# Kernel optimization log

Measured on AMD Instinct MI355X. Metric: run time of the kernel, lower is better.

Reference implementation:

```python
import jax, jax.numpy as jnp
import numpy as np

C = 512
GROUPS = 8
EPS = 1e-5


def setup_inputs() -> dict:
    key = jax.random.key(0)
    ks = jax.random.split(key, 7)
    B, H, W = 16, 32, 32
    x = jax.random.normal(ks[0], (B, C, H, W), dtype=jnp.float32)
    gamma = jnp.ones((C,), jnp.float32)
    beta = jnp.zeros((C,), jnp.float32)
    # 1x1 convs stored as [out, in] matrices
    w_qkv = jax.random.normal(ks[1], (3 * C, C), dtype=jnp.float32) * (1.0 / np.sqrt(C))
    b_qkv = jax.random.normal(ks[2], (3 * C,), dtype=jnp.float32) * 0.02
    w_proj = jax.random.normal(ks[3], (C, C), dtype=jnp.float32) * (1.0 / np.sqrt(C))
    b_proj = jax.random.normal(ks[4], (C,), dtype=jnp.float32) * 0.02
    return {"x": x, "gamma": gamma, "beta": beta, "w_qkv": w_qkv,
            "b_qkv": b_qkv, "w_proj": w_proj, "b_proj": b_proj}


def _group_norm(x, gamma, beta):
    B, Cc, H, W = x.shape
    xg = x.reshape(B, GROUPS, Cc // GROUPS, H, W)
    mean = xg.mean(axis=(2, 3, 4), keepdims=True)
    var = xg.var(axis=(2, 3, 4), keepdims=True)
    xg = (xg - mean) * jax.lax.rsqrt(var + EPS)
    x = xg.reshape(B, Cc, H, W)
    return x * gamma[None, :, None, None] + beta[None, :, None, None]


def reference(x, gamma, beta, w_qkv, b_qkv, w_proj, b_proj):
    B, Cc, H, W = x.shape
    N = H * W
    h = _group_norm(x, gamma, beta)  # [B,C,H,W]
    hf = h.reshape(B, Cc, N)  # [B,C,N]
    # 1x1 conv == matmul over channel dim
    qkv = jnp.einsum('oc,bcn->bon', w_qkv, hf) + b_qkv[None, :, None]  # [B,3C,N]
    q, k, v = jnp.split(qkv, 3, axis=1)  # each [B,C,N]
    scale = 1.0 / jnp.sqrt(jnp.float32(Cc))
    # attn[b,i,j] = sum_c q[b,c,i] * k[b,c,j]
    attn = jnp.einsum('bci,bcj->bij', q, k) * scale  # [B,N,N]
    attn = jax.nn.softmax(attn, axis=-1)
    out = jnp.einsum('bij,bcj->bci', attn, v)  # [B,C,N]
    out = jnp.einsum('oc,bcn->bon', w_proj, out) + b_proj[None, :, None]
    return x + out.reshape(B, Cc, H, W)
```

## Files before the change

kernel.cpp:

```cpp
#include <hip/hip_runtime.h>
#include <hip/hip_bf16.h>

typedef unsigned short u16;
typedef unsigned int u32;
typedef __attribute__((ext_vector_type(8))) short short8;
typedef __attribute__((ext_vector_type(4))) float floatx4;

#define BATCH 16
#define CDIM 512
#define NSPAT 1024
#define NGROUP 8

__device__ __forceinline__ u16 f2bf(float f) {
    unsigned u = __float_as_uint(f);
    u += 0x7FFFu + ((u >> 16) & 1u);
    return (u16)(u >> 16);
}
__device__ __forceinline__ u32 f2bf2(float lo, float hi) {
    __hip_bfloat162 h = __float22bfloat162_rn(make_float2(lo, hi));
    return *(u32*)&h;
}
__device__ __forceinline__ float bf2f(u16 v) {
    u32 t = ((u32)v) << 16;
    return __uint_as_float(t);
}

__device__ __forceinline__ void load_lds16(const void* g, void* l) {
    __builtin_amdgcn_global_load_lds(
        (const __attribute__((address_space(1))) unsigned int*)g,
        (__attribute__((address_space(3))) unsigned int*)l, 16, 0, 0);
}

#define SBAR0 __builtin_amdgcn_sched_barrier(0)
#define BARRIER { SBAR0; __builtin_amdgcn_s_barrier(); SBAR0; }

__global__ __launch_bounds__(256) void prep_kernel(
    const float* __restrict__ w_qkv, const float* __restrict__ w_proj,
    const float* __restrict__ b_qkv, const float* __restrict__ x,
    u16* __restrict__ wproj_bf, u16* __restrict__ wq_t, u16* __restrict__ wk_t,
    u16* __restrict__ wv_t, float* __restrict__ stats, float* __restrict__ lsums,
    float* __restrict__ bpv, float* __restrict__ cvec) {
    int b = blockIdx.x;
    int tid = threadIdx.x;
    if (b < 256) {
        int i = b * 256 + tid;
        float4 v = ((const float4*)w_proj)[i];
        u32* d = (u32*)wproj_bf;
        d[i * 2] = f2bf2(v.x, v.y);
        d[i * 2 + 1] = f2bf2(v.z, v.w);
        return;
    }
    if (b < 448) {
        __shared__ u16 t[64 * 66];
        int bt = b - 256;
        int which = bt >> 6;
        int bt2 = bt & 63;
        int tx = bt2 & 7, ty = bt2 >> 3;
        const float* src = w_qkv + (size_t)(which * 512 + ty * 64) * CDIM + tx * 64;
        u16* dstb = (which == 0) ? wq_t : (which == 1) ? wk_t : wv_t;
#pragma unroll
        for (int p = 0; p < 4; ++p) {
            int r = p * 16 + (tid >> 4);
            int c4 = (tid & 15) << 2;
            float4 v = *(const float4*)(src + (size_t)r * CDIM + c4);
            u16* d = &t[r * 66 + c4];
            d[0] = f2bf(v.x); d[1] = f2bf(v.y); d[2] = f2bf(v.z); d[3] = f2bf(v.w);
        }
        __syncthreads();
        u16* dst = dstb + (size_t)(tx * 64) * CDIM + ty * 64;
#pragma unroll
        for (int p = 0; p < 4; ++p) {
            int c = p * 16 + (tid >> 4);
            int r4 = (tid & 15) << 2;
            ushort4 o;
            o.x = t[(r4 + 0) * 66 + c];
            o.y = t[(r4 + 1) * 66 + c];
            o.z = t[(r4 + 2) * 66 + c];
            o.w = t[(r4 + 3) * 66 + c];
            *(ushort4*)(dst + (size_t)c * CDIM + r4) = o;
        }
        return;
    }
    if (b < 576) {
        __shared__ float rs[4], rss[4];
        int bg = b - 448;
        const float4* xv = (const float4*)(x + (size_t)bg * 65536);
        float s = 0.f, ss = 0.f;
        for (int i = tid; i < 16384; i += 256) {
            float4 v = xv[i];
            s += v.x + v.y + v.z + v.w;
            ss += v.x * v.x + v.y * v.y + v.z * v.z + v.w * v.w;
        }
#pragma unroll
        for (int off = 32; off; off >>= 1) { s += __shfl_down(s, off); ss += __shfl_down(ss, off); }
        int wave = tid >> 6, lane = tid & 63;
        if (lane == 0) { rs[wave] = s; rss[wave] = ss; }
        __syncthreads();
        if (tid == 0) {
            float S1 = rs[0] + rs[1] + rs[2] + rs[3];
            float S2 = rss[0] + rss[1] + rss[2] + rss[3];
            float mean = S1 * (1.f / 65536.f);
            float var = S2 * (1.f / 65536.f) - mean * mean;
            stats[bg * 2] = mean;
            stats[bg * 2 + 1] = rsqrtf(var + 1e-5f);
        }
        return;
    }
    if (b < 592) {
        ((float4*)lsums)[(b - 576) * 256 + tid] = (float4){0.f, 0.f, 0.f, 0.f};
        return;
    }
    if (b < 600) {
        int o0 = (b - 592) * 64;
        int wave = tid >> 6, lane = tid & 63;
        const float4* bvv = (const float4*)(b_qkv + 1024);
        float4 v0 = bvv[lane * 2], v1 = bvv[lane * 2 + 1];
        for (int it = 0; it < 16; ++it) {
            int o = o0 + wave * 16 + it;
            const float4* wr = (const float4*)(w_proj + (size_t)o * CDIM);
            float4 a0 = wr[lane * 2], a1 = wr[lane * 2 + 1];
            float s = a0.x * v0.x + a0.y * v0.y + a0.z * v0.z + a0.w * v0.w
                    + a1.x * v1.x + a1.y * v1.y + a1.z * v1.z + a1.w * v1.w;
#pragma unroll
            for (int off = 32; off; off >>= 1) s += __shfl_down(s, off);
            if (lane == 0) bpv[o] = s;
        }
        return;
    }
    {
        int col = (b - 600) * 256 + tid;
        float s = 0.f;
        for (int m = 0; m < 512; ++m)
            s += w_qkv[(size_t)(512 + m) * CDIM + col] * b_qkv[m];
        cvec[col] = s;
    }
}

__device__ __forceinline__ void stage_tile(
    const u16* __restrict__ Ab, const u16* __restrict__ Bb, int lda, int ldb,
    int m0, int n0, int k0, u16* As, u16* Bs) {
    int tid = threadIdx.x;
#pragma unroll
    for (int it = 0; it < 4; ++it) {
        int c = it * 256 + tid;
        int r = c >> 3, p = c & 7;
        int kc = p ^ (r & 7);
        load_lds16(Ab + (size_t)(m0 + r) * lda + k0 + (kc << 3), &As[c << 3]);
        load_lds16(Bb + (size_t)(n0 + r) * ldb + k0 + (kc << 3), &Bs[c << 3]);
    }
}

__device__ __forceinline__ void compute_tile(
    const u16* As, const u16* Bs, int wm, int wn, int quad, int lrow,
    floatx4 (&acc)[4][4]) {
#pragma unroll
    for (int s = 0; s < 2; ++s) {
        short8 af[4], bf[4];
#pragma unroll
        for (int i = 0; i < 4; ++i) {
            int R = wm + i * 16 + lrow;
            int p = (s * 4 + quad) ^ (R & 7);
            af[i] = *(const short8*)&As[(R << 6) + (p << 3)];
        }
#pragma unroll
        for (int j = 0; j < 4; ++j) {
            int R = wn + j * 16 + lrow;
            int p = (s * 4 + quad) ^ (R & 7);
            bf[j] = *(const short8*)&Bs[(R << 6) + (p << 3)];
        }
#pragma unroll
        for (int i = 0; i < 4; ++i)
#pragma unroll
            for (int j = 0; j < 4; ++j)
                acc[i][j] = __builtin_amdgcn_mfma_f32_16x16x32_bf16(af[i], bf[j], acc[i][j], 0, 0, 0);
    }
}

__device__ __forceinline__ void gemm_core_sb(
    const u16* __restrict__ Ab, const u16* __restrict__ Bb, int K, int lda, int ldb,
    int m0, int n0, u16* As, u16* Bs, floatx4 (&acc)[4][4]) {
    int tid = threadIdx.x;
    int lane = tid & 63, wave = tid >> 6, quad = lane >> 4, lrow = lane & 15;
    int wm = (wave >> 1) << 6, wn = (wave & 1) << 6;
    for (int k0 = 0; k0 < K; k0 += 64) {
        stage_tile(Ab, Bb, lda, ldb, m0, n0, k0, As, Bs);
        __syncthreads();
        compute_tile(As, Bs, wm, wn, quad, lrow, acc);
        __syncthreads();
    }
}

#define ACC_INIT floatx4 acc[4][4]; \
    _Pragma("unroll") for (int i = 0; i < 4; ++i) \
    _Pragma("unroll") for (int j = 0; j < 4; ++j) acc[i][j] = (floatx4){0.f, 0.f, 0.f, 0.f};

#define EPILOG_IDX int lane = threadIdx.x & 63, wave = threadIdx.x >> 6; \
    int quad = lane >> 4, lrow = lane & 15; \
    int wm = (wave >> 1) << 6, wn = (wave & 1) << 6;

__device__ __forceinline__ void issueA2(
    const u16* __restrict__ Ab, int lda, int m0, int t, int h, u16* smem) {
    int tid = threadIdx.x;
    u16* base = smem + (t & 1) * 16384 + h * 8192;
#pragma unroll
    for (int l = 0; l < 2; ++l) {
        int c = l * 512 + tid;
        int rho = c >> 3, p = c & 7;
        int kc = p ^ (rho & 7);
        int r = ((rho >> 6) << 7) | (h << 6) | (rho & 63);
        load_lds16(Ab + (size_t)(m0 + r) * lda + (t << 6) + (kc << 3), base + (c << 3));
    }
}
__device__ __forceinline__ void issueB2(
    const u16* __restrict__ Bb, int ldb, int n0, int t, int h, u16* smem) {
    int tid = threadIdx.x;
    u16* base = smem + 32768 + (t & 1) * 16384 + h * 8192;
#pragma unroll
    for (int l = 0; l < 2; ++l) {
        int c = l * 512 + tid;
        int rho = c >> 3, p = c & 7;
        int kc = p ^ (rho & 7);
        int r = ((rho >> 5) << 6) | (h << 5) | (rho & 31);
        load_lds16(Bb + (size_t)(n0 + r) * ldb + (t << 6) + (kc << 3), base + (c << 3));
    }
}

__device__ __forceinline__ void gemm256x256(
    const u16* __restrict__ Ab, const u16* __restrict__ Bb, int K, int lda, int ldb,
    int m0, int n0, u16* smem, floatx4 (&acc)[8][4]) {
    int tid = threadIdx.x;
    int lane = tid & 63, wave = tid >> 6;
    int quad = lane >> 4, lrow = lane & 15;
    int wrow = wave >> 2, wcol = wave & 3;
    int nt = K >> 6;
    issueA2(Ab, lda, m0, 0, 0, smem);
    issueA2(Ab, lda, m0, 0, 1, smem);
    issueB2(Bb, ldb, n0, 0, 0, smem);
    issueB2(Bb, ldb, n0, 0, 1, smem);
    for (int t = 0; t < nt; ++t) {
        int slot = t & 1;
        BARRIER;
        if (t + 1 < nt) {
            issueA2(Ab, lda, m0, t + 1, 0, smem);
            issueA2(Ab, lda, m0, t + 1, 1, smem);
            issueB2(Bb, ldb, n0, t + 1, 0, smem);
            issueB2(Bb, ldb, n0, t + 1, 1, smem);
            asm volatile("s_waitcnt vmcnt(8)" ::: "memory");
        } else {
            asm volatile("s_waitcnt vmcnt(0)" ::: "memory");
        }
        BARRIER;
        const u16* Ah = smem + slot * 16384;
        const u16* Bh = smem + 32768 + slot * 16384;
        short8 bf[2][4];
#pragma unroll
        for (int qn = 0; qn < 2; ++qn)
#pragma unroll
            for (int ks = 0; ks < 2; ++ks)
#pragma unroll
                for (int j = 0; j < 2; ++j) {
                    int rho = wcol * 32 + j * 16 + lrow;
                    int p = (ks * 4 + quad) ^ (lrow & 7);
                    bf[qn][ks * 2 + j] = *(const short8*)&Bh[qn * 8192 + (rho << 6) + (p << 3)];
                }
#pragma unroll
        for (int qm = 0; qm < 2; ++qm) {
            short8 af[8];
#pragma unroll
            for (int ks = 0; ks < 2; ++ks)
#pragma unroll
                for (int i = 0; i < 4; ++i) {
                    int rho = wrow * 64 + i * 16 + lrow;
                    int p = (ks * 4 + quad) ^ (lrow & 7);
                    af[ks * 4 + i] = *(const short8*)&Ah[qm * 8192 + (rho << 6) + (p << 3)];
                }
#pragma unroll
            for (int ks = 0; ks < 2; ++ks)
#pragma unroll
                for (int i = 0; i < 4; ++i)
#pragma unroll
                    for (int qn = 0; qn < 2; ++qn)
#pragma unroll
                        for (int j = 0; j < 2; ++j)
                            acc[qm * 4 + i][qn * 2 + j] = __builtin_amdgcn_mfma_f32_16x16x32_bf16(
                                af[ks * 4 + i], bf[qn][ks * 2 + j], acc[qm * 4 + i][qn * 2 + j], 0, 0, 0);
        }
    }
}

__device__ __forceinline__ void issueA4(
    const u16* __restrict__ Ab, int lda, int m0, int t, u16* smem) {
    int tid = threadIdx.x;
    u16* base = smem + (t & 1) * 16384;
#pragma unroll
    for (int l = 0; l < 4; ++l) {
        int c = l * 512 + tid;
        int rho = c >> 3, p = c & 7;
        int kc = p ^ (rho & 7);
        load_lds16(Ab + (size_t)(m0 + rho) * lda + (t << 6) + (kc << 3), base + (c << 3));
    }
}
__device__ __forceinline__ void issueB4(
    const u16* __restrict__ Bb, int ldb, int n0, int t, int h, u16* smem) {
    int tid = threadIdx.x;
    u16* base = smem + 32768 + (t & 1) * 8192 + h * 4096;
    int rho = tid >> 3, p = tid & 7;
    int kc = p ^ (rho & 7);
    int r = ((rho >> 5) << 6) | (h << 5) | (rho & 31);
    load_lds16(Bb + (size_t)(n0 + r) * ldb + (t << 6) + (kc << 3), base + (tid << 3));
}

__device__ __forceinline__ void gemm256x128(
    const u16* __restrict__ Ab, const u16* __restrict__ Bb, int K, int lda, int ldb,
    int m0, int n0, u16* smem, floatx4 (&acc)[4][4]) {
    int tid = threadIdx.x;
    int lane = tid & 63, wave = tid >> 6;
    int quad = lane >> 4, lrow = lane & 15;
    int wrow = wave >> 1, wcol = wave & 1;
    int nt = K >> 6;
    issueA4(Ab, lda, m0, 0, smem);
    issueB4(Bb, ldb, n0, 0, 0, smem);
    issueB4(Bb, ldb, n0, 0, 1, smem);
    for (int t = 0; t < nt; ++t) {
        int slot = t & 1;
        BARRIER;
        if (t + 1 < nt) {
            issueA4(Ab, lda, m0, t + 1, smem);
            issueB4(Bb, ldb, n0, t + 1, 0, smem);
            issueB4(Bb, ldb, n0, t + 1, 1, smem);
            asm volatile("s_waitcnt vmcnt(6)" ::: "memory");
        } else {
            asm volatile("s_waitcnt vmcnt(0)" ::: "memory");
        }
        BARRIER;
        const u16* Ah = smem + slot * 16384;
        const u16* Bh = smem + 32768 + slot * 8192;
        short8 bf[2][4];
#pragma unroll
        for (int qn = 0; qn < 2; ++qn)
#pragma unroll
            for (int ks = 0; ks < 2; ++ks)
#pragma unroll
                for (int j = 0; j < 2; ++j) {
                    int rho = wcol * 32 + j * 16 + lrow;
                    int p = (ks * 4 + quad) ^ (lrow & 7);
                    bf[qn][ks * 2 + j] = *(const short8*)&Bh[qn * 4096 + (rho << 6) + (p << 3)];
                }
        short8 af[8];
#pragma unroll
        for (int ks = 0; ks < 2; ++ks)
#pragma unroll
            for (int i = 0; i < 4; ++i) {
                int rho = wrow * 64 + i * 16 + lrow;
                int p = (ks * 4 + quad) ^ (lrow & 7);
                af[ks * 4 + i] = *(const short8*)&Ah[(rho << 6) + (p << 3)];
            }
#pragma unroll
        for (int ks = 0; ks < 2; ++ks)
#pragma unroll
            for (int i = 0; i < 4; ++i)
#pragma unroll
                for (int qn = 0; qn < 2; ++qn)
#pragma unroll
                    for (int j = 0; j < 2; ++j)
                        acc[i][qn * 2 + j] = __builtin_amdgcn_mfma_f32_16x16x32_bf16(
                            af[ks * 4 + i], bf[qn][ks * 2 + j], acc[i][qn * 2 + j], 0, 0, 0);
    }
}

#define ACC_INIT84 floatx4 acc[8][4]; \
    _Pragma("unroll") for (int i = 0; i < 8; ++i) \
    _Pragma("unroll") for (int j = 0; j < 4; ++j) acc[i][j] = (floatx4){0.f, 0.f, 0.f, 0.f};

#define ACC_INIT44 floatx4 acc[4][4]; \
    _Pragma("unroll") for (int i = 0; i < 4; ++i) \
    _Pragma("unroll") for (int j = 0; j < 4; ++j) acc[i][j] = (floatx4){0.f, 0.f, 0.f, 0.f};

#define TSTR 66
__global__ __launch_bounds__(256) void gn_wpv_kernel(
    const float* __restrict__ x, const float* __restrict__ gamma, const float* __restrict__ beta,
    const float* __restrict__ stats, u16* __restrict__ hT,
    const u16* __restrict__ wproj_bf, const u16* __restrict__ wq_t,
    const u16* __restrict__ wk_t, const u16* __restrict__ wv_t, u16* __restrict__ wmega) {
    __shared__ u16 smem[2 * 128 * 64];
    int tid = threadIdx.x;
    if (blockIdx.z == 16) {
        if (blockIdx.x >= 4) return;
        bool isM = blockIdx.y < 4;
        int m0 = (isM ? blockIdx.y : blockIdx.y - 4) << 7;
        int n0 = blockIdx.x << 7;
        const u16* Aop = isM ? wq_t : wproj_bf;
        const u16* Bop = isM ? wk_t : wv_t;
        int rbase = isM ? 0 : 512;
        ACC_INIT;
        gemm_core_sb(Aop, Bop, CDIM, CDIM, CDIM, m0, n0, smem, smem + 128 * 64, acc);
        EPILOG_IDX;
#pragma unroll
        for (int i = 0; i < 4; ++i)
#pragma unroll
            for (int j = 0; j < 4; ++j)
#pragma unroll
                for (int r = 0; r < 4; ++r) {
                    int R = m0 + wm + i * 16 + (quad << 2) + r;
                    int Cc = n0 + wn + j * 16 + lrow;
                    wmega[(size_t)(rbase + R) * CDIM + Cc] = f2bf(acc[i][j][r]);
                }
        return;
    }
    u16* t = smem;
    int b = blockIdx.z, c0 = blockIdx.y << 6, n0 = blockIdx.x << 6;
    const float* xb = x + ((size_t)b * CDIM + c0) * NSPAT + n0;
#pragma unroll
    for (int p = 0; p < 4; ++p) {
        int cl = p * 16 + (tid >> 4);
        int nl = (tid & 15) << 2;
        int c = c0 + cl;
        int bg = b * NGROUP + (c >> 6);
        float ga = gamma[c] * stats[bg * 2 + 1];
        float be = beta[c] - stats[bg * 2] * ga;
        float4 v = *(const float4*)(xb + (size_t)cl * NSPAT + nl);
        u16* dst = &t[cl * TSTR + nl];
        dst[0] = f2bf(v.x * ga + be);
        dst[1] = f2bf(v.y * ga + be);
        dst[2] = f2bf(v.z * ga + be);
        dst[3] = f2bf(v.w * ga + be);
    }
    __syncthreads();
    u16* hb = hT + ((size_t)b * NSPAT + n0) * CDIM + c0;
#pragma unroll
    for (int p = 0; p < 4; ++p) {
        int nl = p * 16 + (tid >> 4);
        int cl4 = (tid & 15) << 2;
        ushort4 o;
        o.x = t[(cl4 + 0) * TSTR + nl];
        o.y = t[(cl4 + 1) * TSTR + nl];
        o.z = t[(cl4 + 2) * TSTR + nl];
        o.w = t[(cl4 + 3) * TSTR + nl];
        *(ushort4*)(hb + (size_t)nl * CDIM + cl4) = o;
    }
}

__global__ __launch_bounds__(512, 2) void qkv_kernel(
    const u16* __restrict__ wmega, const u16* __restrict__ hT,
    const float* __restrict__ cvec, const float* __restrict__ bpv,
    u16* __restrict__ gT, u16* __restrict__ WV, float* __restrict__ rbuf) {
    extern __shared__ u16 smem[];
    int z = blockIdx.x;
    if (blockIdx.y == 4) {
        if (blockIdx.z != 0) return;
        int tid = threadIdx.x;
        const u16* hb = hT + (size_t)z * CDIM * NSPAT;
#pragma unroll 1
        for (int jj = 0; jj < 2; ++jj) {
            int j = tid * 2 + jj;
            const short8* hp = (const short8*)(hb + (size_t)j * CDIM);
            float s = 0.f;
#pragma unroll 4
            for (int cc = 0; cc < 64; ++cc) {
                short8 v = hp[cc];
                const float4* cv = (const float4*)&cvec[cc * 8];
                float4 c0 = cv[0], c1 = cv[1];
                s += c0.x * bf2f((u16)v[0]) + c0.y * bf2f((u16)v[1])
                   + c0.z * bf2f((u16)v[2]) + c0.w * bf2f((u16)v[3])
                   + c1.x * bf2f((u16)v[4]) + c1.y * bf2f((u16)v[5])
                   + c1.z * bf2f((u16)v[6]) + c1.w * bf2f((u16)v[7]);
            }
            rbuf[(size_t)z * NSPAT + j] = s;
        }
        return;
    }
    int n0 = blockIdx.y << 8;
    int m0 = blockIdx.z << 8;
    const u16* Bb = hT + (size_t)z * CDIM * NSPAT;
    ACC_INIT84;
    gemm256x256(wmega, Bb, CDIM, CDIM, CDIM, m0, n0, smem, acc);
    int lane = threadIdx.x & 63, wave = threadIdx.x >> 6;
    int quad = lane >> 4, lrow = lane & 15;
    int wrow = wave >> 2, wcol = wave & 3;
    if (blockIdx.z < 2) {
        u16* gp = gT + (size_t)z * NSPAT * CDIM;
#pragma unroll
        for (int mf = 0; mf < 8; ++mf) {
            int R0 = m0 + wrow * 128 + mf * 16 + (quad << 2);
#pragma unroll
            for (int nf = 0; nf < 4; ++nf) {
                int Cc = n0 + wcol * 64 + nf * 16 + lrow;
                uint2 u;
                u.x = f2bf2(acc[mf][nf][0], acc[mf][nf][1]);
                u.y = f2bf2(acc[mf][nf][2], acc[mf][nf][3]);
                *(uint2*)&gp[(size_t)Cc * CDIM + R0] = u;
            }
        }
    } else {
        u16* Wp = WV + (size_t)z * CDIM * NSPAT;
#pragma unroll
        for (int mf = 0; mf < 8; ++mf) {
            int R = m0 - 512 + wrow * 128 + mf * 16 + (quad << 2);
            float4 pv = *(const float4*)&bpv[R];
#pragma unroll
            for (int nf = 0; nf < 4; ++nf) {
                int Cc = n0 + wcol * 64 + nf * 16 + lrow;
                Wp[(size_t)(R + 0) * NSPAT + Cc] = f2bf(acc[mf][nf][0] + pv.x);
                Wp[(size_t)(R + 1) * NSPAT + Cc] = f2bf(acc[mf][nf][1] + pv.y);
                Wp[(size_t)(R + 2) * NSPAT + Cc] = f2bf(acc[mf][nf][2] + pv.z);
                Wp[(size_t)(R + 3) * NSPAT + Cc] = f2bf(acc[mf][nf][3] + pv.w);
            }
        }
    }
}

__global__ __launch_bounds__(512, 2) void scores_kernel(
    const u16* __restrict__ gT, const u16* __restrict__ hT,
    u16* __restrict__ P, float* __restrict__ lsums, const float* __restrict__ rbuf,
    float scale) {
    extern __shared__ u16 smem[];
    int z = blockIdx.x;
    int n0 = blockIdx.y << 8;
    int m0 = blockIdx.z << 8;
    const u16* gb = gT + (size_t)z * NSPAT * CDIM;
    const u16* hb = hT + (size_t)z * CDIM * NSPAT;
    ACC_INIT84;
    gemm256x256(gb, hb, CDIM, CDIM, CDIM, m0, n0, smem, acc);
    int lane = threadIdx.x & 63, wave = threadIdx.x >> 6;
    int quad = lane >> 4, lrow = lane & 15;
    int wrow = wave >> 2, wcol = wave & 3;
    u16* Pp = P + (size_t)z * NSPAT * NSPAT;
    float* ls = lsums + (size_t)z * NSPAT;
    const float* rb = rbuf + (size_t)z * NSPAT;
#pragma unroll
    for (int nf = 0; nf < 4; ++nf) {
        int Ci = n0 + wcol * 64 + nf * 16 + lrow;
        float part = 0.f;
#pragma unroll
        for (int mf = 0; mf < 8; ++mf) {
            int Rj0 = m0 + wrow * 128 + mf * 16 + (quad << 2);
            float4 rv = *(const float4*)&rb[Rj0];
            float e0 = __expf((acc[mf][nf][0] + rv.x) * scale);
            float e1 = __expf((acc[mf][nf][1] + rv.y) * scale);
            float e2 = __expf((acc[mf][nf][2] + rv.z) * scale);
            float e3 = __expf((acc[mf][nf][3] + rv.w) * scale);
            part += (e0 + e1) + (e2 + e3);
            uint2 u;
            u.x = f2bf2(e0, e1);
            u.y = f2bf2(e2, e3);
            *(uint2*)&Pp[(size_t)Ci * NSPAT + Rj0] = u;
        }
        part += __shfl_xor(part, 16);
        part += __shfl_xor(part, 32);
        if (lane < 16) atomicAdd(&ls[Ci], part);
    }
}

__global__ __launch_bounds__(512, 2) void final_kernel(
    const u16* __restrict__ WV, const u16* __restrict__ P, const float* __restrict__ lsums,
    const float* __restrict__ bias, const float* __restrict__ x, float* __restrict__ out) {
    extern __shared__ u16 smem[];
    int z = blockIdx.x;
    int n0 = blockIdx.y << 7;
    int m0 = blockIdx.z << 8;
    const u16* Pb = P + (size_t)z * NSPAT * NSPAT;
    const u16* WVb = WV + (size_t)z * CDIM * NSPAT;
    ACC_INIT44;
    gemm256x128(Pb, WVb, NSPAT, NSPAT, NSPAT, m0, n0, smem, acc);
    int lane = threadIdx.x & 63, wave = threadIdx.x >> 6;
    int quad = lane >> 4, lrow = lane & 15;
    int wrow = wave >> 1, wcol = wave & 1;
    float* Op = out + (size_t)z * CDIM * NSPAT;
    const float* xr = x + (size_t)z * CDIM * NSPAT;
    const float* li = lsums + (size_t)z * NSPAT;
#pragma unroll
    for (int mf = 0; mf < 4; ++mf) {
        int Ri0 = m0 + wrow * 64 + mf * 16 + (quad << 2);
        float4 lv = *(const float4*)&li[Ri0];
        float s0 = __builtin_amdgcn_rcpf(lv.x);
        float s1 = __builtin_amdgcn_rcpf(lv.y);
        float s2 = __builtin_amdgcn_rcpf(lv.z);
        float s3 = __builtin_amdgcn_rcpf(lv.w);
#pragma unroll
        for (int nf = 0; nf < 4; ++nf) {
            int Co = n0 + wcol * 64 + nf * 16 + lrow;
            float bv = bias[Co];
            size_t off = (size_t)Co * NSPAT + Ri0;
            float4 xv = *(const float4*)&xr[off];
            float4 o;
            o.x = acc[mf][nf][0] * s0 + bv + xv.x;
            o.y = acc[mf][nf][1] * s1 + bv + xv.y;
            o.z = acc[mf][nf][2] * s2 + bv + xv.z;
            o.w = acc[mf][nf][3] * s3 + bv + xv.w;
            *(float4*)&Op[off] = o;
        }
    }
}

extern "C" void kernel_launch(void* const* d_in, const int* in_sizes, int n_in,
                              void* d_out, int out_size, void* d_ws, size_t ws_size,
                              hipStream_t stream) {
    const float* x      = (const float*)d_in[0];
    const float* gamma  = (const float*)d_in[1];
    const float* beta   = (const float*)d_in[2];
    const float* w_qkv  = (const float*)d_in[3];
    const float* b_qkv  = (const float*)d_in[4];
    const float* w_proj = (const float*)d_in[5];
    const float* b_proj = (const float*)d_in[6];
    float* out = (float*)d_out;

    const size_t CN = (size_t)CDIM * NSPAT;
    const size_t NN = (size_t)NSPAT * NSPAT;
    const float SCALE = 0.044194173824159216f;
    const int LDS_BIG = 131072;
    const int LDS_MED = 98304;

    static bool lds_attr_done = false;
    if (!lds_attr_done) {
        hipFuncSetAttribute((const void*)qkv_kernel,
                            hipFuncAttributeMaxDynamicSharedMemorySize, LDS_BIG);
        hipFuncSetAttribute((const void*)scores_kernel,
                            hipFuncAttributeMaxDynamicSharedMemorySize, LDS_BIG);
        hipFuncSetAttribute((const void*)final_kernel,
                            hipFuncAttributeMaxDynamicSharedMemorySize, LDS_MED);
        lds_attr_done = true;
    }

    char* ws = (char*)d_ws;
    float* stats   = (float*)ws;
    float* bpv     = (float*)(ws + 1024);
    float* cvec    = (float*)(ws + 3072);
    u16* wmega     = (u16*)(ws + 8192);
    u16* wproj_bf  = wmega + (size_t)1024 * CDIM;
    u16* wq_t      = wproj_bf + (size_t)CDIM * CDIM;
    u16* wk_t      = wq_t + (size_t)CDIM * CDIM;
    u16* wv_t      = wk_t + (size_t)CDIM * CDIM;
    u16* hT        = wv_t + (size_t)CDIM * CDIM;
    u16* gT        = hT + BATCH * CN;
    u16* WV        = gT + BATCH * CN;
    u16* P         = WV + BATCH * CN;
    float* lsums   = (float*)(P + BATCH * NN);
    float* rbuf    = lsums + (size_t)BATCH * NSPAT;

    prep_kernel<<<602, 256, 0, stream>>>(
        w_qkv, w_proj, b_qkv, x, wproj_bf, wq_t, wk_t, wv_t, stats, lsums, bpv, cvec);

    gn_wpv_kernel<<<dim3(16, 8, 17), 256, 0, stream>>>(
        x, gamma, beta, stats, hT, wproj_bf, wq_t, wk_t, wv_t, wmega);

    qkv_kernel<<<dim3(BATCH, 5, 4), 512, LDS_BIG, stream>>>(
        wmega, hT, cvec, bpv, gT, WV, rbuf);

    scores_kernel<<<dim3(BATCH, 4, 4), 512, LDS_BIG, stream>>>(
        gT, hT, P, lsums, rbuf, SCALE);

    final_kernel<<<dim3(BATCH, 4, 4), 512, LDS_MED, stream>>>(WV, P, lsums, b_proj, x, out);
}
```

Baseline: 136.6 us.

## Fuse rbuf row-bias reduction into group-norm transpose kernel via atomics

Moves the per-position dot product of cvec with the normalized activations out of a dedicated slice of the qkv kernel and into the group-norm/transpose kernel. There it is computed from the bf16 tile already held in shared memory and accumulated into rbuf with atomicAdd. The prep kernel gets extra blocks to zero rbuf alongside lsums. This removes the serial, low-parallelism rbuf blocks from the qkv grid and a second read of hT, at the cost of an extra barrier and global atomics in the transpose kernel. The atomic accumulation order is nondeterministic.

New measurement: 128.8 us. 1.06x faster.

```diff
diff --git a/kernel.cpp b/kernel.cpp
--- a/kernel.cpp
+++ b/kernel.cpp
@@ -106,12 +106,12 @@
         }
         return;
     }
-    if (b < 592) {
+    if (b < 608) {
         ((float4*)lsums)[(b - 576) * 256 + tid] = (float4){0.f, 0.f, 0.f, 0.f};
         return;
     }
-    if (b < 600) {
-        int o0 = (b - 592) * 64;
+    if (b < 616) {
+        int o0 = (b - 608) * 64;
         int wave = tid >> 6, lane = tid & 63;
         const float4* bvv = (const float4*)(b_qkv + 1024);
         float4 v0 = bvv[lane * 2], v1 = bvv[lane * 2 + 1];
@@ -128,7 +128,7 @@
         return;
     }
     {
-        int col = (b - 600) * 256 + tid;
+        int col = (b - 616) * 256 + tid;
         float s = 0.f;
         for (int m = 0; m < 512; ++m)
             s += w_qkv[(size_t)(512 + m) * CDIM + col] * b_qkv[m];
@@ -381,8 +381,10 @@
     const float* __restrict__ x, const float* __restrict__ gamma, const float* __restrict__ beta,
     const float* __restrict__ stats, u16* __restrict__ hT,
     const u16* __restrict__ wproj_bf, const u16* __restrict__ wq_t,
-    const u16* __restrict__ wk_t, const u16* __restrict__ wv_t, u16* __restrict__ wmega) {
+    const u16* __restrict__ wk_t, const u16* __restrict__ wv_t, u16* __restrict__ wmega,
+    const float* __restrict__ cvec, float* __restrict__ rbuf) {
     __shared__ u16 smem[2 * 128 * 64];
+    __shared__ float rp[4][64];
     int tid = threadIdx.x;
     if (blockIdx.z == 16) {
         if (blockIdx.x >= 4) return;
@@ -426,6 +428,21 @@
         dst[3] = f2bf(v.w * ga + be);
     }
     __syncthreads();
+    {
+        int j = tid & 63, part = tid >> 6;
+        float rs_ = 0.f;
+#pragma unroll
+        for (int q = 0; q < 16; ++q) {
+            int cl = part * 16 + q;
+            rs_ += cvec[c0 + cl] * bf2f(t[cl * TSTR + j]);
+        }
+        rp[part][j] = rs_;
+    }
+    __syncthreads();
+    if (tid < 64) {
+        float s = rp[0][tid] + rp[1][tid] + rp[2][tid] + rp[3][tid];
+        atomicAdd(&rbuf[(size_t)b * NSPAT + n0 + tid], s);
+    }
     u16* hb = hT + ((size_t)b * NSPAT + n0) * CDIM + c0;
 #pragma unroll
     for (int p = 0; p < 4; ++p) {
@@ -442,33 +459,10 @@
 
 __global__ __launch_bounds__(512, 2) void qkv_kernel(
     const u16* __restrict__ wmega, const u16* __restrict__ hT,
-    const float* __restrict__ cvec, const float* __restrict__ bpv,
-    u16* __restrict__ gT, u16* __restrict__ WV, float* __restrict__ rbuf) {
+    const float* __restrict__ bpv,
+    u16* __restrict__ gT, u16* __restrict__ WV) {
     extern __shared__ u16 smem[];
     int z = blockIdx.x;
-    if (blockIdx.y == 4) {
-        if (blockIdx.z != 0) return;
-        int tid = threadIdx.x;
-        const u16* hb = hT + (size_t)z * CDIM * NSPAT;
-#pragma unroll 1
-        for (int jj = 0; jj < 2; ++jj) {
-            int j = tid * 2 + jj;
-            const short8* hp = (const short8*)(hb + (size_t)j * CDIM);
-            float s = 0.f;
-#pragma unroll 4
-            for (int cc = 0; cc < 64; ++cc) {
-                short8 v = hp[cc];
-                const float4* cv = (const float4*)&cvec[cc * 8];
-                float4 c0 = cv[0], c1 = cv[1];
-                s += c0.x * bf2f((u16)v[0]) + c0.y * bf2f((u16)v[1])
-                   + c0.z * bf2f((u16)v[2]) + c0.w * bf2f((u16)v[3])
-                   + c1.x * bf2f((u16)v[4]) + c1.y * bf2f((u16)v[5])
-                   + c1.z * bf2f((u16)v[6]) + c1.w * bf2f((u16)v[7]);
-            }
-            rbuf[(size_t)z * NSPAT + j] = s;
-        }
-        return;
-    }
     int n0 = blockIdx.y << 8;
     int m0 = blockIdx.z << 8;
     const u16* Bb = hT + (size_t)z * CDIM * NSPAT;
@@ -637,14 +631,14 @@
     float* lsums   = (float*)(P + BATCH * NN);
     float* rbuf    = lsums + (size_t)BATCH * NSPAT;
 
-    prep_kernel<<<602, 256, 0, stream>>>(
+    prep_kernel<<<618, 256, 0, stream>>>(
         w_qkv, w_proj, b_qkv, x, wproj_bf, wq_t, wk_t, wv_t, stats, lsums, bpv, cvec);
 
     gn_wpv_kernel<<<dim3(16, 8, 17), 256, 0, stream>>>(
-        x, gamma, beta, stats, hT, wproj_bf, wq_t, wk_t, wv_t, wmega);
-
-    qkv_kernel<<<dim3(BATCH, 5, 4), 512, LDS_BIG, stream>>>(
-        wmega, hT, cvec, bpv, gT, WV, rbuf);
+        x, gamma, beta, stats, hT, wproj_bf, wq_t, wk_t, wv_t, wmega, cvec, rbuf);
+
+    qkv_kernel<<<dim3(BATCH, 4, 4), 512, LDS_BIG, stream>>>(
+        wmega, hT, bpv, gT, WV);
 
     scores_kernel<<<dim3(BATCH, 4, 4), 512, LDS_BIG, stream>>>(
         gT, hT, P, lsums, rbuf, SCALE);
```
